# Optimization experiments

Hardware: AMD Instinct MI355X
Metric: run time of the kernel (lower is better)

## Reference

```python
import jax, jax.numpy as jnp
import numpy as np

N_NODES = 50000
N_EDGES = 800000
HIDDEN = 128
OUT = 128


def setup_inputs() -> dict:
    key = jax.random.key(0)
    k1, k2, k3, k4, k5, k6 = jax.random.split(key, 6)
    h = jax.random.normal(k1, (N_NODES, HIDDEN), dtype=jnp.float32)
    src = jax.random.randint(k2, (N_EDGES,), 0, N_NODES, dtype=jnp.int64)
    dst = jax.random.randint(k3, (N_EDGES,), 0, N_NODES, dtype=jnp.int64)
    scale = 1.0 / np.sqrt(HIDDEN)
    W_edge = jax.random.normal(k4, (OUT, HIDDEN), dtype=jnp.float32) * scale
    W_self = jax.random.normal(k5, (OUT, HIDDEN), dtype=jnp.float32) * scale
    b_self = jax.random.normal(k6, (OUT,), dtype=jnp.float32) * scale
    return {"h": h, "src": src, "dst": dst, "W_edge": W_edge, "W_self": W_self, "b_self": b_self}


def reference(h, src, dst, W_edge, W_self, b_self):
    n = h.shape[0]
    # edge_transform(src_features): same linear on every edge -> transform nodes once, then gather
    msg_node = h @ W_edge.T                       # [N, OUT]
    msg = msg_node[src]                           # [E, OUT] gather
    sums = jax.ops.segment_sum(msg, dst, num_segments=n)  # [N, OUT] scatter-add
    deg = jax.ops.segment_sum(jnp.ones((dst.shape[0],), dtype=h.dtype), dst, num_segments=n)
    h1 = sums / jnp.maximum(deg, 1.0)[:, None]    # mean; zero in-degree -> 0 (DGL semantics)
    out = jax.nn.relu(h @ W_self.T + b_self + h1)
    return out
```

## Files before the change

kernel.cpp:

```cpp
#include <hip/hip_runtime.h>

#define N_HID 128
#define CAP   64
#define OVF_CAP 8192

typedef short bf16x8 __attribute__((ext_vector_type(8)));
typedef float f32x4  __attribute__((ext_vector_type(4)));

static __device__ __forceinline__ unsigned short f2bf(float f)
{
    unsigned int u = __float_as_uint(f);
    u = (u + 0x7fffu + ((u >> 16) & 1u)) >> 16;
    return (unsigned short)u;
}
static __device__ __forceinline__ float bf2f(unsigned int bits16)
{
    return __uint_as_float(bits16 << 16);
}

__global__ __launch_bounds__(256) void fragmentize(
    const float* __restrict__ h,
    const float* __restrict__ We,
    const float* __restrict__ Ws,
    unsigned short* __restrict__ Ah,
    unsigned short* __restrict__ Be,
    unsigned short* __restrict__ Bs,
    int n, int nrt)
{
    int b = blockIdx.x;
    const float* src; unsigned short* dstF; int rt, nrows;
    if (b < nrt)          { src = h;  dstF = Ah; rt = b;           nrows = n;   }
    else if (b < nrt + 8) { src = We; dstF = Be; rt = b - nrt;     nrows = 128; }
    else                  { src = Ws; dstF = Bs; rt = b - nrt - 8; nrows = 128; }

    int t  = threadIdx.x;
    int kc = t >> 6;
    int l  = t & 63;
    int m  = l & 15;
    int q  = l >> 4;

    int row = rt * 16 + m;
    if (row > nrows - 1) row = nrows - 1;

    const float* p = &src[(size_t)row * N_HID + kc * 32 + q * 8];
    float4 v0 = *(const float4*)p;
    float4 v1 = *(const float4*)(p + 4);

    uint4 pk;
    pk.x = (unsigned int)f2bf(v0.x) | ((unsigned int)f2bf(v0.y) << 16);
    pk.y = (unsigned int)f2bf(v0.z) | ((unsigned int)f2bf(v0.w) << 16);
    pk.z = (unsigned int)f2bf(v1.x) | ((unsigned int)f2bf(v1.y) << 16);
    pk.w = (unsigned int)f2bf(v1.z) | ((unsigned int)f2bf(v1.w) << 16);

    *(uint4*)&dstF[(size_t)rt * 2048 + kc * 512 + l * 8] = pk;
}

__global__ __launch_bounds__(256) void gemm_mfma(
    const unsigned short* __restrict__ Afrag,
    const unsigned short* __restrict__ Bfrag,
    const float* __restrict__ bias,
    unsigned short* __restrict__ msgOut,
    float* __restrict__ fOut,
    int n, int nrt)
{
    int w = (int)((blockIdx.x * blockDim.x + threadIdx.x) >> 6);
    if (w >= nrt) return;
    int l = threadIdx.x & 63;

    const bf16x8* Ap = (const bf16x8*)(Afrag + (size_t)w * 2048);
    bf16x8 a0 = Ap[l], a1 = Ap[64 + l], a2 = Ap[128 + l], a3 = Ap[192 + l];

    const int m0   = w * 16;
    const int colb = l & 15;
    const int rq   = (l >> 4) * 4;

#pragma unroll
    for (int ct = 0; ct < 8; ++ct) {
        const bf16x8* Bp = (const bf16x8*)(Bfrag + (size_t)ct * 2048);
        f32x4 acc = {0.f, 0.f, 0.f, 0.f};
        acc = __builtin_amdgcn_mfma_f32_16x16x32_bf16(a0, Bp[l],       acc, 0, 0, 0);
        acc = __builtin_amdgcn_mfma_f32_16x16x32_bf16(a1, Bp[64 + l],  acc, 0, 0, 0);
        acc = __builtin_amdgcn_mfma_f32_16x16x32_bf16(a2, Bp[128 + l], acc, 0, 0, 0);
        acc = __builtin_amdgcn_mfma_f32_16x16x32_bf16(a3, Bp[192 + l], acc, 0, 0, 0);

        int col = ct * 16 + colb;
        if (bias) {
            float bv = bias[col];
#pragma unroll
            for (int r = 0; r < 4; ++r) {
                int row = m0 + rq + r;
                if (row < n) fOut[(size_t)row * N_HID + col] = acc[r] + bv;
            }
        } else {
#pragma unroll
            for (int r = 0; r < 4; ++r) {
                int row = m0 + rq + r;
                if (row < n) msgOut[(size_t)row * N_HID + col] = f2bf(acc[r]);
            }
        }
    }
}

__global__ void bucket_scatter(const int* __restrict__ src,
                               const int* __restrict__ dst,
                               int* __restrict__ cnt,
                               int* __restrict__ bucket,
                               int* __restrict__ ovfn,
                               long long* __restrict__ ovf,
                               int E)
{
    int e = blockIdx.x * blockDim.x + threadIdx.x;
    if (e < E) {
        int d = dst[e];
        int s = src[e];
        int c = atomicAdd(&cnt[d], 1);
        if (c < CAP) {
            bucket[(size_t)d * CAP + c] = s;
        } else {
            int o = atomicAdd(ovfn, 1);
            if (o < OVF_CAP) ovf[o] = ((long long)d << 32) | (unsigned int)s;
        }
    }
}

__global__ __launch_bounds__(256) void gather_finish(
    const int* __restrict__ cnt,
    const int* __restrict__ bucket,
    const int* __restrict__ ovfn,
    const long long* __restrict__ ovf,
    const unsigned short* __restrict__ msg,
    float* __restrict__ out,
    int n)
{
    int node = blockIdx.x * 4 + (threadIdx.x >> 6);
    if (node >= n) return;
    int lane = threadIdx.x & 63;
    int deg  = cnt[node];
    int m    = deg < CAP ? deg : CAP;

    const int* bk = &bucket[(size_t)node * CAP];
    const unsigned int* m32 = (const unsigned int*)msg;

    float ax = 0.f, ay = 0.f;
    int i = 0;
    for (; i + 4 <= m; i += 4) {
        int s0 = bk[i + 0], s1 = bk[i + 1], s2 = bk[i + 2], s3 = bk[i + 3];
        unsigned int v0 = m32[(size_t)s0 * 64 + lane];
        unsigned int v1 = m32[(size_t)s1 * 64 + lane];
        unsigned int v2 = m32[(size_t)s2 * 64 + lane];
        unsigned int v3 = m32[(size_t)s3 * 64 + lane];
        ax += bf2f(v0 & 0xffffu) + bf2f(v1 & 0xffffu) + bf2f(v2 & 0xffffu) + bf2f(v3 & 0xffffu);
        ay += bf2f(v0 >> 16)     + bf2f(v1 >> 16)     + bf2f(v2 >> 16)     + bf2f(v3 >> 16);
    }
    for (; i < m; ++i) {
        unsigned int v = m32[(size_t)bk[i] * 64 + lane];
        ax += bf2f(v & 0xffffu);
        ay += bf2f(v >> 16);
    }

    if (deg > CAP) {
        int no = *ovfn; if (no > OVF_CAP) no = OVF_CAP;
        for (int o = 0; o < no; ++o) {
            long long pk = ovf[o];
            if ((int)(pk >> 32) == node) {
                unsigned int v = m32[(size_t)(unsigned int)pk * 64 + lane];
                ax += bf2f(v & 0xffffu);
                ay += bf2f(v >> 16);
            }
        }
    }

    float sc = deg > 0 ? 1.0f / (float)deg : 0.f;

    float2* o2 = (float2*)out;
    float2 sv  = o2[(size_t)node * 64 + lane];
    float2 r;
    r.x = fmaxf(sv.x + ax * sc, 0.f);
    r.y = fmaxf(sv.y + ay * sc, 0.f);
    o2[(size_t)node * 64 + lane] = r;
}

extern "C" void kernel_launch(void* const* d_in, const int* in_sizes, int n_in,
                              void* d_out, int out_size, void* d_ws, size_t ws_size,
                              hipStream_t stream)
{
    const float* h   = (const float*)d_in[0];
    const int*   src = (const int*)d_in[1];
    const int*   dst = (const int*)d_in[2];
    const float* We  = (const float*)d_in[3];
    const float* Ws  = (const float*)d_in[4];
    const float* bs  = (const float*)d_in[5];
    float*       out = (float*)d_out;

    const int n   = in_sizes[0] / N_HID;
    const int E   = in_sizes[1];
    const int nrt = (n + 15) / 16;

    unsigned short* msg = (unsigned short*)d_ws;
    unsigned short* Ah  = msg + (size_t)n * N_HID;
    int*            bucket = (int*)Ah;
    unsigned short* Be  = Ah + (size_t)nrt * 2048;
    unsigned short* Bs  = Be + 8 * 2048;
    int*  cnt  = (int*)(Bs + 8 * 2048);
    int*  ovfn = cnt + n;
    long long* ovf = (long long*)(ovfn + 8);

    hipMemsetAsync(cnt, 0, sizeof(int) * (size_t)(n + 8), stream);
    fragmentize<<<nrt + 16, 256, 0, stream>>>(h, We, Ws, Ah, Be, Bs, n, nrt);
    gemm_mfma<<<(nrt + 3) / 4, 256, 0, stream>>>(Ah, Be, nullptr, msg, nullptr, n, nrt);
    gemm_mfma<<<(nrt + 3) / 4, 256, 0, stream>>>(Ah, Bs, bs, nullptr, out, n, nrt);
    bucket_scatter<<<(E + 255) / 256, 256, 0, stream>>>(src, dst, cnt, bucket, ovfn, ovf, E);
    gather_finish<<<(n + 3) / 4, 256, 0, stream>>>(cnt, bucket, ovfn, ovf, msg, out, n);
}
```

Measured before the change: 196.5 us.

## Merge GEMM launches and partition edge scatter by destination slice per XCD

Combines the two node GEMMs into one launch that selects the weight matrix by block index. Rewrites the bucket scatter so each block, via blockIdx mod 8, handles only destinations in one eighth of the node range while scanning a chunk of edges. The aim is to keep atomics and bucket writes for a node range local to one XCD's L2 and reduce cross-die coherence traffic. In exchange, each dst index is read eight times and the number of blocks is fixed.

```diff
diff --git a/kernel.cpp b/kernel.cpp
--- a/kernel.cpp
+++ b/kernel.cpp
@@ -55,17 +55,23 @@
     *(uint4*)&dstF[(size_t)rt * 2048 + kc * 512 + l * 8] = pk;
 }
 
-__global__ __launch_bounds__(256) void gemm_mfma(
+__global__ __launch_bounds__(256) void gemm_mfma2(
     const unsigned short* __restrict__ Afrag,
-    const unsigned short* __restrict__ Bfrag,
+    const unsigned short* __restrict__ Be,
+    const unsigned short* __restrict__ Bsf,
     const float* __restrict__ bias,
     unsigned short* __restrict__ msgOut,
     float* __restrict__ fOut,
-    int n, int nrt)
-{
-    int w = (int)((blockIdx.x * blockDim.x + threadIdx.x) >> 6);
+    int n, int nrt, int nwb)
+{
+    int b    = blockIdx.x;
+    bool sp  = b >= nwb;
+    int bl   = sp ? b - nwb : b;
+    int w    = bl * 4 + ((int)threadIdx.x >> 6);
     if (w >= nrt) return;
     int l = threadIdx.x & 63;
+
+    const unsigned short* Bfrag = sp ? Bsf : Be;
 
     const bf16x8* Ap = (const bf16x8*)(Afrag + (size_t)w * 2048);
     bf16x8 a0 = Ap[l], a1 = Ap[64 + l], a2 = Ap[128 + l], a3 = Ap[192 + l];
@@ -84,7 +90,7 @@
         acc = __builtin_amdgcn_mfma_f32_16x16x32_bf16(a3, Bp[192 + l], acc, 0, 0, 0);
 
         int col = ct * 16 + colb;
-        if (bias) {
+        if (sp) {
             float bv = bias[col];
 #pragma unroll
             for (int r = 0; r < 4; ++r) {
@@ -101,24 +107,36 @@
     }
 }
 
-__global__ void bucket_scatter(const int* __restrict__ src,
-                               const int* __restrict__ dst,
-                               int* __restrict__ cnt,
-                               int* __restrict__ bucket,
-                               int* __restrict__ ovfn,
-                               long long* __restrict__ ovf,
-                               int E)
-{
-    int e = blockIdx.x * blockDim.x + threadIdx.x;
-    if (e < E) {
+__global__ __launch_bounds__(256) void bucket_scatter(
+    const int* __restrict__ src,
+    const int* __restrict__ dst,
+    int* __restrict__ cnt,
+    int* __restrict__ bucket,
+    int* __restrict__ ovfn,
+    long long* __restrict__ ovf,
+    int E, int n)
+{
+    const int slice = blockIdx.x & 7;
+    const int g     = blockIdx.x >> 3;
+    const int nG    = (int)(gridDim.x >> 3);
+    const int lo    = (int)(((long long)slice * n) / 8);
+    const int hi    = (int)(((long long)(slice + 1) * n) / 8);
+
+    const int chunk = (E + nG - 1) / nG;
+    const int e0 = g * chunk;
+    const int e1 = (e0 + chunk < E) ? e0 + chunk : E;
+
+    for (int e = e0 + (int)threadIdx.x; e < e1; e += 256) {
         int d = dst[e];
-        int s = src[e];
-        int c = atomicAdd(&cnt[d], 1);
-        if (c < CAP) {
-            bucket[(size_t)d * CAP + c] = s;
-        } else {
-            int o = atomicAdd(ovfn, 1);
-            if (o < OVF_CAP) ovf[o] = ((long long)d << 32) | (unsigned int)s;
+        if (d >= lo && d < hi) {
+            int s = src[e];
+            int c = atomicAdd(&cnt[d], 1);
+            if (c < CAP) {
+                bucket[(size_t)d * CAP + c] = s;
+            } else {
+                int o = atomicAdd(ovfn, 1);
+                if (o < OVF_CAP) ovf[o] = ((long long)d << 32) | (unsigned int)s;
+            }
         }
     }
 }
@@ -195,6 +213,7 @@
     const int n   = in_sizes[0] / N_HID;
     const int E   = in_sizes[1];
     const int nrt = (n + 15) / 16;
+    const int nwb = (nrt + 3) / 4;
 
     unsigned short* msg = (unsigned short*)d_ws;
     unsigned short* Ah  = msg + (size_t)n * N_HID;
@@ -207,8 +226,7 @@
 
     hipMemsetAsync(cnt, 0, sizeof(int) * (size_t)(n + 8), stream);
     fragmentize<<<nrt + 16, 256, 0, stream>>>(h, We, Ws, Ah, Be, Bs, n, nrt);
-    gemm_mfma<<<(nrt + 3) / 4, 256, 0, stream>>>(Ah, Be, nullptr, msg, nullptr, n, nrt);
-    gemm_mfma<<<(nrt + 3) / 4, 256, 0, stream>>>(Ah, Bs, bs, nullptr, out, n, nrt);
-    bucket_scatter<<<(E + 255) / 256, 256, 0, stream>>>(src, dst, cnt, bucket, ovfn, ovf, E);
+    gemm_mfma2<<<2 * nwb, 256, 0, stream>>>(Ah, Be, Bs, bs, msg, out, n, nrt, nwb);
+    bucket_scatter<<<512, 256, 0, stream>>>(src, dst, cnt, bucket, ovfn, ovf, E, n);
     gather_finish<<<(n + 3) / 4, 256, 0, stream>>>(cnt, bucket, ovfn, ovf, msg, out, n);
 }
```

Measured after the change: 189.2 us. -3.7%, faster.
